# Performance work log

Hardware: AMD Instinct MI355X
Metric: run time of the kernel (lower is better)

The kernel has to match this reference:

```python
import jax, jax.numpy as jnp
import numpy as np

D = 1024
L_COMP = 16384
L_FULL = 32768
EPS = 1e-4


def setup_inputs() -> dict:
    key = jax.random.key(0)
    k1, k2 = jax.random.split(key)
    x = jax.random.normal(k1, (1, L_COMP, D), dtype=jnp.float32)
    p_selected = jax.random.uniform(k2, (L_COMP,), dtype=jnp.float32)
    # boundary mask over full sequence: exactly L_COMP ones, first position forced to 1
    rng = np.random.default_rng(0)
    pos = np.concatenate([[0], np.sort(rng.choice(np.arange(1, L_FULL), L_COMP - 1, replace=False))])
    b_np = np.zeros((1, L_FULL), dtype=np.int32)
    b_np[0, pos] = 1
    b = jnp.asarray(b_np)
    return {"x": x, "p_selected": p_selected, "b": b}


def _ema_scan(x, p):
    # z_t = (1 - p_t) * z_{t-1} + p_t * x_t  (exact math of the mamba chunk scan
    # with A=-1, dt=log(1/(1-p)), B=p, C=1, x pre-divided by dt)
    a = jnp.broadcast_to((1.0 - p)[None, :, None], x.shape)  # (1, L, d) decay
    bxt = p[None, :, None] * x                                # (1, L, d) input term

    def combine(c1, c2):
        a1, b1 = c1
        a2, b2 = c2
        return a1 * a2, a2 * b1 + b2

    _, z = jax.lax.associative_scan(combine, (a, bxt), axis=1)
    return z


def reference(x, p_selected, b):
    p = jnp.clip(p_selected.astype(jnp.float32), EPS, 1.0 - EPS)  # (L_comp,)
    z_bar = _ema_scan(x.astype(jnp.float32), p)                   # (1, L_comp, d)
    plug_back_idx = jnp.cumsum(b, axis=1) - 1                     # (1, L_full)
    out = jnp.take(z_bar[0], plug_back_idx[0], axis=0)[None]      # (1, L_full, d)
    return out.astype(x.dtype)
```

## Files before the change

### kernel.cpp

```cpp
#include <hip/hip_runtime.h>


#define DCH 1024
#define L_COMP 16384
#define L_FULL 32768
#define CHUNK 32
#define NCHUNK (L_COMP / CHUNK)
#define SEG (L_FULL / NCHUNK)
#define EPSV 1e-4f

__device__ __forceinline__ float clipp(float p) {
    p = fmaxf(p, EPSV);
    p = fminf(p, 1.0f - EPSV);
    return p;
}

__global__ __launch_bounds__(256, 2) void chunk_kernel(
    const float* __restrict__ x, const float* __restrict__ p,
    const int* __restrict__ b,
    float* __restrict__ Bbuf, float* __restrict__ Abuf, int* __restrict__ bsum) {
    const int c = blockIdx.x;
    const int tid = threadIdx.x;
    const int lane = tid & 63;
    const int wave = tid >> 6;
    const int base = c * CHUNK;

    const float4* x4 = reinterpret_cast<const float4*>(x) + (size_t)c * CHUNK * (DCH / 4) + tid;
    float4 h = make_float4(0.f, 0.f, 0.f, 0.f);
    float aprod = 1.0f;
    for (int ib = 0; ib < CHUNK; ib += 8) {
        float4 xv[8];
        float pv[8];
#pragma unroll
        for (int j = 0; j < 8; ++j) {
            xv[j] = x4[(ib + j) * (DCH / 4)];
            pv[j] = clipp(p[base + ib + j]);
        }
#pragma unroll
        for (int j = 0; j < 8; ++j) {
            float a = 1.0f - pv[j];
            h.x = fmaf(a, h.x, pv[j] * xv[j].x);
            h.y = fmaf(a, h.y, pv[j] * xv[j].y);
            h.z = fmaf(a, h.z, pv[j] * xv[j].z);
            h.w = fmaf(a, h.w, pv[j] * xv[j].w);
            aprod *= a;
        }
    }
    reinterpret_cast<float4*>(Bbuf)[c * (DCH / 4) + tid] = h;
    if (tid == 0) Abuf[c] = aprod;
    if (wave == 0) {
        int v = b[c * SEG + lane];
        int s = v;
#pragma unroll
        for (int off = 1; off < 64; off <<= 1) s += __shfl_xor(s, off, 64);
        if (lane == 0) bsum[c] = s;
    }
}

__global__ __launch_bounds__(256, 2) void dechunk_kernel(
    const float* __restrict__ x, const float* __restrict__ p,
    const int* __restrict__ b, float* __restrict__ out,
    const float* __restrict__ Bbuf, const float* __restrict__ Abuf,
    const int* __restrict__ bsum) {
    const int c = blockIdx.x;
    const int tid = threadIdx.x;
    const int lane = tid & 63;
    const int wave = tid >> 6;
    const int base = c * CHUNK;

    __shared__ int bpref[NCHUNK + 1];
    __shared__ int spos[CHUNK + 1];
    __shared__ int wtot[4];

    {
        int v0 = bsum[2 * tid];
        int v1 = bsum[2 * tid + 1];
        int s = v0 + v1;
        int incl = s;
#pragma unroll
        for (int off = 1; off < 64; off <<= 1) {
            int n = __shfl_up(incl, off, 64);
            if (lane >= off) incl += n;
        }
        if (lane == 63) wtot[wave] = incl;
        __syncthreads();
        int woff = 0;
        for (int w = 0; w < wave; ++w) woff += wtot[w];
        int ex = woff + incl - s;
        bpref[2 * tid] = ex;
        bpref[2 * tid + 1] = ex + v0;
        if (tid == 0) bpref[NCHUNK] = L_COMP;
        __syncthreads();
    }

    if (tid <= CHUNK) {
        int t = base + tid;
        int posv = L_FULL;
        if (t < L_COMP) {
            int lo = 0, hi = NCHUNK;
            while (hi - lo > 1) {
                int mid = (lo + hi) >> 1;
                if (bpref[mid] <= t) lo = mid; else hi = mid;
            }
            int lr = t - bpref[lo];
            const int4* bseg = reinterpret_cast<const int4*>(b) + lo * (SEG / 4);
            int cnt = 0;
#pragma unroll 4
            for (int q = 0; q < SEG / 4; ++q) {
                int4 w = bseg[q];
                if (w.x) { if (cnt == lr) posv = lo * SEG + 4 * q + 0; ++cnt; }
                if (w.y) { if (cnt == lr) posv = lo * SEG + 4 * q + 1; ++cnt; }
                if (w.z) { if (cnt == lr) posv = lo * SEG + 4 * q + 2; ++cnt; }
                if (w.w) { if (cnt == lr) posv = lo * SEG + 4 * q + 3; ++cnt; }
            }
        }
        spos[tid] = posv;
    }

    float4 h = make_float4(0.f, 0.f, 0.f, 0.f);
    {
        const float4* B4 = reinterpret_cast<const float4*>(Bbuf) + tid;
        int k = 0;
        for (; k + 16 <= c; k += 16) {
            float4 bv[16];
            float av[16];
#pragma unroll
            for (int j = 0; j < 16; ++j) {
                bv[j] = B4[(k + j) * (DCH / 4)];
                av[j] = Abuf[k + j];
            }
#pragma unroll
            for (int j = 0; j < 16; ++j) {
                h.x = fmaf(av[j], h.x, bv[j].x);
                h.y = fmaf(av[j], h.y, bv[j].y);
                h.z = fmaf(av[j], h.z, bv[j].z);
                h.w = fmaf(av[j], h.w, bv[j].w);
            }
        }
        for (; k < c; ++k) {
            float4 bv = B4[k * (DCH / 4)];
            float a = Abuf[k];
            h.x = fmaf(a, h.x, bv.x);
            h.y = fmaf(a, h.y, bv.y);
            h.z = fmaf(a, h.z, bv.z);
            h.w = fmaf(a, h.w, bv.w);
        }
    }
    __syncthreads();

    {
        const float4* x4 = reinterpret_cast<const float4*>(x) + (size_t)c * CHUNK * (DCH / 4) + tid;
        float4* out4 = reinterpret_cast<float4*>(out) + tid;
        int f0 = spos[0];
        for (int ib = 0; ib < CHUNK; ib += 8) {
            float4 xv[8];
            float pv[8];
            int fe[8];
#pragma unroll
            for (int j = 0; j < 8; ++j) {
                xv[j] = x4[(ib + j) * (DCH / 4)];
                pv[j] = clipp(p[base + ib + j]);
                fe[j] = spos[ib + j + 1];
            }
#pragma unroll
            for (int j = 0; j < 8; ++j) {
                float a = 1.0f - pv[j];
                h.x = fmaf(a, h.x, pv[j] * xv[j].x);
                h.y = fmaf(a, h.y, pv[j] * xv[j].y);
                h.z = fmaf(a, h.z, pv[j] * xv[j].z);
                h.w = fmaf(a, h.w, pv[j] * xv[j].w);
                for (int f = f0; f < fe[j]; ++f) {
                    out4[(size_t)f * (DCH / 4)] = h;
                }
                f0 = fe[j];
            }
        }
    }
}

extern "C" void kernel_launch(void* const* d_in, const int* in_sizes, int n_in,
                              void* d_out, int out_size, void* d_ws, size_t ws_size,
                              hipStream_t stream) {
    const float* x = (const float*)d_in[0];
    const float* p = (const float*)d_in[1];
    const int* b = (const int*)d_in[2];
    float* out = (float*)d_out;

    char* ws = (char*)d_ws;
    float* Abuf = (float*)ws;
    int* bsum = (int*)(ws + 4096);
    float* Bbuf = (float*)(ws + 8192);

    chunk_kernel<<<NCHUNK, 256, 0, stream>>>(x, p, b, Bbuf, Abuf, bsum);
    dechunk_kernel<<<NCHUNK, 256, 0, stream>>>(x, p, b, out, Bbuf, Abuf, bsum);
}
```

Measured before the change: 226.0 us.

## Replace per-block quadratic inter-chunk prefix with a dedicated sequential carry kernel

Previously each dechunk block recomputed its incoming state by scanning all earlier chunk summaries, so the total work and L2 traffic grew quadratically with the number of chunks. A new small kernel now scans the chunk summaries once, in order, and writes the carry-in state for every chunk to a workspace buffer. Dechunk then reads a single carry vector per block. It also switches x loads and output stores to nontemporal hints. The cost is an extra launch and a serial 512-step scan run by only four small blocks, which is latency-bound.

```diff
diff --git a/kernel.cpp b/kernel.cpp
--- a/kernel.cpp
+++ b/kernel.cpp
@@ -8,6 +8,8 @@
 #define NCHUNK (L_COMP / CHUNK)
 #define SEG (L_FULL / NCHUNK)
 #define EPSV 1e-4f
+
+typedef float v4f __attribute__((ext_vector_type(4)));
 
 __device__ __forceinline__ float clipp(float p) {
     p = fmaxf(p, EPSV);
@@ -25,11 +27,11 @@
     const int wave = tid >> 6;
     const int base = c * CHUNK;
 
-    const float4* x4 = reinterpret_cast<const float4*>(x) + (size_t)c * CHUNK * (DCH / 4) + tid;
-    float4 h = make_float4(0.f, 0.f, 0.f, 0.f);
+    const v4f* x4 = reinterpret_cast<const v4f*>(x) + (size_t)c * CHUNK * (DCH / 4) + tid;
+    v4f h = (v4f)0.f;
     float aprod = 1.0f;
     for (int ib = 0; ib < CHUNK; ib += 8) {
-        float4 xv[8];
+        v4f xv[8];
         float pv[8];
 #pragma unroll
         for (int j = 0; j < 8; ++j) {
@@ -39,14 +41,11 @@
 #pragma unroll
         for (int j = 0; j < 8; ++j) {
             float a = 1.0f - pv[j];
-            h.x = fmaf(a, h.x, pv[j] * xv[j].x);
-            h.y = fmaf(a, h.y, pv[j] * xv[j].y);
-            h.z = fmaf(a, h.z, pv[j] * xv[j].z);
-            h.w = fmaf(a, h.w, pv[j] * xv[j].w);
+            h = a * h + pv[j] * xv[j];
             aprod *= a;
         }
     }
-    reinterpret_cast<float4*>(Bbuf)[c * (DCH / 4) + tid] = h;
+    reinterpret_cast<v4f*>(Bbuf)[c * (DCH / 4) + tid] = h;
     if (tid == 0) Abuf[c] = aprod;
     if (wave == 0) {
         int v = b[c * SEG + lane];
@@ -57,11 +56,34 @@
     }
 }
 
+#define BATCHB 32
+__global__ __launch_bounds__(64) void interchunk_kernel(
+    const float* __restrict__ Bbuf, const float* __restrict__ Abuf,
+    float* __restrict__ Hbuf) {
+    const int ch4 = blockIdx.x * 64 + threadIdx.x;
+    const v4f* B4 = reinterpret_cast<const v4f*>(Bbuf) + ch4;
+    v4f* H4 = reinterpret_cast<v4f*>(Hbuf) + ch4;
+    v4f h = (v4f)0.f;
+    for (int cb = 0; cb < NCHUNK; cb += BATCHB) {
+        v4f bv[BATCHB];
+        float av[BATCHB];
+#pragma unroll
+        for (int j = 0; j < BATCHB; ++j) {
+            bv[j] = B4[(cb + j) * (DCH / 4)];
+            av[j] = Abuf[cb + j];
+        }
+#pragma unroll
+        for (int j = 0; j < BATCHB; ++j) {
+            H4[(cb + j) * (DCH / 4)] = h;
+            h = av[j] * h + bv[j];
+        }
+    }
+}
+
 __global__ __launch_bounds__(256, 2) void dechunk_kernel(
     const float* __restrict__ x, const float* __restrict__ p,
     const int* __restrict__ b, float* __restrict__ out,
-    const float* __restrict__ Bbuf, const float* __restrict__ Abuf,
-    const int* __restrict__ bsum) {
+    const float* __restrict__ Hbuf, const int* __restrict__ bsum) {
     const int c = blockIdx.x;
     const int tid = threadIdx.x;
     const int lane = tid & 63;
@@ -116,61 +138,29 @@
         }
         spos[tid] = posv;
     }
-
-    float4 h = make_float4(0.f, 0.f, 0.f, 0.f);
-    {
-        const float4* B4 = reinterpret_cast<const float4*>(Bbuf) + tid;
-        int k = 0;
-        for (; k + 16 <= c; k += 16) {
-            float4 bv[16];
-            float av[16];
-#pragma unroll
-            for (int j = 0; j < 16; ++j) {
-                bv[j] = B4[(k + j) * (DCH / 4)];
-                av[j] = Abuf[k + j];
-            }
-#pragma unroll
-            for (int j = 0; j < 16; ++j) {
-                h.x = fmaf(av[j], h.x, bv[j].x);
-                h.y = fmaf(av[j], h.y, bv[j].y);
-                h.z = fmaf(av[j], h.z, bv[j].z);
-                h.w = fmaf(av[j], h.w, bv[j].w);
-            }
-        }
-        for (; k < c; ++k) {
-            float4 bv = B4[k * (DCH / 4)];
-            float a = Abuf[k];
-            h.x = fmaf(a, h.x, bv.x);
-            h.y = fmaf(a, h.y, bv.y);
-            h.z = fmaf(a, h.z, bv.z);
-            h.w = fmaf(a, h.w, bv.w);
-        }
-    }
     __syncthreads();
 
     {
-        const float4* x4 = reinterpret_cast<const float4*>(x) + (size_t)c * CHUNK * (DCH / 4) + tid;
-        float4* out4 = reinterpret_cast<float4*>(out) + tid;
+        const v4f* x4 = reinterpret_cast<const v4f*>(x) + (size_t)c * CHUNK * (DCH / 4) + tid;
+        v4f* out4 = reinterpret_cast<v4f*>(out) + tid;
+        v4f h = reinterpret_cast<const v4f*>(Hbuf)[c * (DCH / 4) + tid];
         int f0 = spos[0];
         for (int ib = 0; ib < CHUNK; ib += 8) {
-            float4 xv[8];
+            v4f xv[8];
             float pv[8];
             int fe[8];
 #pragma unroll
             for (int j = 0; j < 8; ++j) {
-                xv[j] = x4[(ib + j) * (DCH / 4)];
+                xv[j] = __builtin_nontemporal_load(&x4[(ib + j) * (DCH / 4)]);
                 pv[j] = clipp(p[base + ib + j]);
                 fe[j] = spos[ib + j + 1];
             }
 #pragma unroll
             for (int j = 0; j < 8; ++j) {
                 float a = 1.0f - pv[j];
-                h.x = fmaf(a, h.x, pv[j] * xv[j].x);
-                h.y = fmaf(a, h.y, pv[j] * xv[j].y);
-                h.z = fmaf(a, h.z, pv[j] * xv[j].z);
-                h.w = fmaf(a, h.w, pv[j] * xv[j].w);
+                h = a * h + pv[j] * xv[j];
                 for (int f = f0; f < fe[j]; ++f) {
-                    out4[(size_t)f * (DCH / 4)] = h;
+                    __builtin_nontemporal_store(h, &out4[(size_t)f * (DCH / 4)]);
                 }
                 f0 = fe[j];
             }
@@ -190,7 +180,9 @@
     float* Abuf = (float*)ws;
     int* bsum = (int*)(ws + 4096);
     float* Bbuf = (float*)(ws + 8192);
+    float* Hbuf = Bbuf + (size_t)NCHUNK * DCH;
 
     chunk_kernel<<<NCHUNK, 256, 0, stream>>>(x, p, b, Bbuf, Abuf, bsum);
-    dechunk_kernel<<<NCHUNK, 256, 0, stream>>>(x, p, b, out, Bbuf, Abuf, bsum);
+    interchunk_kernel<<<4, 64, 0, stream>>>(Bbuf, Abuf, Hbuf);
+    dechunk_kernel<<<NCHUNK, 256, 0, stream>>>(x, p, b, out, Hbuf, bsum);
 }
```

Result: slower. 239.0 us (+5.8%).
